# Kernel tuning notes

Measured on AMD Instinct MI355X. Metric: run time of the kernel, lower is better.

## Reference

```python
import jax, jax.numpy as jnp
import numpy as np

M_BIT = 8      # BfpConfig.bfp_M_Bit (sign + mantissa bits)
BLOCK = 64     # BFP block size along contraction (K) dim
K_SIZE, STRIDE, PAD = 3, 1, 1


def bfp_quantize(x, m_bit=M_BIT, block=BLOCK):
    """Block-floating-point quantize along last axis: per-block shared exponent
    from max-abs, m_bit-wide signed mantissa, then dequantize back to fp."""
    shape = x.shape
    xb = x.reshape(shape[:-1] + (shape[-1] // block, block))
    maxabs = jnp.max(jnp.abs(xb), axis=-1, keepdims=True)
    exp = jnp.floor(jnp.log2(jnp.maximum(maxabs, jnp.float32(1e-38))))
    scale = jnp.exp2(exp - (m_bit - 2))          # lsb weight for this block
    qmax = jnp.float32(2.0 ** (m_bit - 1) - 1)
    q = jnp.clip(jnp.round(xb / scale), -qmax - 1.0, qmax) * scale
    q = jnp.where(maxabs == 0.0, 0.0, q)
    return q.reshape(shape)


def im2col(x, k, s, p):
    """Torch Unfold ordering: columns flattened as (C, kh, kw). x: [N,C,H,W]."""
    N, C, H, W = x.shape
    Ho = (H + 2 * p - k) // s + 1
    Wo = (W + 2 * p - k) // s + 1
    xp = jnp.pad(x, ((0, 0), (0, 0), (p, p), (p, p)))
    rows = []
    for i in range(k):
        for j in range(k):
            rows.append(xp[:, :, i:i + s * Ho:s, j:j + s * Wo:s])  # [N,C,Ho,Wo]
    # [k*k, N, C, Ho, Wo] -> [N, C, k*k, Ho*Wo] -> [N, C*k*k, Ho*Wo]
    patches = jnp.stack(rows, axis=0).transpose(1, 2, 0, 3, 4)
    return patches.reshape(N, C * k * k, Ho * Wo), Ho, Wo


def setup_inputs() -> dict:
    key = jax.random.key(0)
    k1, k2, k3 = jax.random.split(key, 3)
    inputs = jax.random.normal(k1, (32, 128, 56, 56), dtype=jnp.float32)
    fan_in = 128 * K_SIZE * K_SIZE
    weight = jax.random.normal(k2, (256, 128, K_SIZE, K_SIZE), dtype=jnp.float32) / np.sqrt(fan_in)
    bias = jax.random.normal(k3, (256,), dtype=jnp.float32) * 0.01
    return {"inputs": inputs, "weight": weight, "bias": bias}


def reference(inputs, weight, bias):
    N = inputs.shape[0]
    C_out = weight.shape[0]
    cols, Ho, Wo = im2col(inputs, K_SIZE, STRIDE, PAD)      # [N, K, Ho*Wo]
    a = cols.transpose(0, 2, 1).reshape(-1, cols.shape[1])  # [N*Ho*Wo, K]
    w = weight.reshape(C_out, -1)                           # [C_out, K]
    qa = bfp_quantize(a)
    qw = bfp_quantize(w)
    out = qa @ qw.T + bias                                  # [N*Ho*Wo, C_out]
    out = out.reshape(N, Ho, Wo, C_out).transpose(0, 3, 1, 2)
    return out
```

## Files before the change

kernel.cpp:

```cpp
#include <hip/hip_runtime.h>

typedef short short8 __attribute__((ext_vector_type(8)));
typedef __bf16 bf16x8 __attribute__((ext_vector_type(8)));
typedef float floatx4 __attribute__((ext_vector_type(4)));

__device__ __forceinline__ float make_pow2(int e) {
  return __builtin_bit_cast(float, (unsigned)((e + 127) << 23));
}

__device__ __forceinline__ void barrier_lgkm() {
  asm volatile("s_waitcnt lgkmcnt(0)" ::: "memory");
  __builtin_amdgcn_sched_barrier(0);
  __builtin_amdgcn_s_barrier();
  asm volatile("" ::: "memory");
  __builtin_amdgcn_sched_barrier(0);
}

__global__ void quant_w_kernel(const float* __restrict__ w, unsigned short* __restrict__ qw) {
  int b = blockIdx.x;
  int ct = b / 18, kb = b - ct * 18;
  int L = threadIdx.x;
  int co = ct * 16 + (L & 15);
  int kq = L >> 4;
  const float* wr = w + co * 1152 + kb * 64 + kq * 8;
  float v[16];
  float a = 0.f;
  #pragma unroll
  for (int ks = 0; ks < 2; ++ks)
    #pragma unroll
    for (int j = 0; j < 8; ++j) {
      float t = wr[ks * 32 + j];
      v[ks * 8 + j] = t;
      a = fmaxf(a, fabsf(t));
    }
  a = fmaxf(a, __shfl_xor(a, 16));
  a = fmaxf(a, __shfl_xor(a, 32));
  short8 q0 = (short8)0, q1 = (short8)0;
  if (a > 0.f) {
    int e = (int)((__builtin_bit_cast(unsigned, a) >> 23) & 0xffu) - 127;
    if (e < -126) e = -126;
    float inv = make_pow2(6 - e);
    float s   = make_pow2(e - 6);
    #pragma unroll
    for (int u = 0; u < 16; ++u) {
      float r = rintf(v[u] * inv);
      r = fminf(fmaxf(r, -128.f), 127.f);
      float qq = r * s;
      unsigned short hb = (unsigned short)(__builtin_bit_cast(unsigned, qq) >> 16);
      if (u < 8) q0[u] = (short)hb; else q1[u - 8] = (short)hb;
    }
  }
  unsigned short* dst = qw + (size_t)(ct * 18 + kb) * 1024;
  *(short8*)(dst + L * 8) = q0;
  *(short8*)(dst + 512 + L * 8) = q1;
}

__global__ __launch_bounds__(512, 4) void conv_bfp_kernel(
    const float* __restrict__ in, const unsigned short* __restrict__ qw,
    const float* __restrict__ bias, float* __restrict__ out) {
  __shared__ unsigned short As[2][64 * 64];
  __shared__ float pmax[2][8][64];

  const int bid = blockIdx.x;
  const int mt = (bid & 7) * 196 + (bid >> 3);
  const int t = threadIdx.x;
  const int lane = t & 63;
  const int wave = __builtin_amdgcn_readfirstlane(t >> 6);

  const unsigned m = mt * 64u + lane;
  const unsigned nimg = m / 3136u;
  const unsigned py = m - nimg * 3136u;
  const int y = (int)(py / 56u);
  const int x = (int)(py - (unsigned)y * 56u);
  const int vbase = (int)((nimg * 401408u + (unsigned)y * 56u + (unsigned)x) * 4u);
  int vm = 0;
  #pragma unroll
  for (int i = 0; i < 3; ++i)
    #pragma unroll
    for (int j = 0; j < 3; ++j)
      if ((unsigned)(y + i - 1) < 56u && (unsigned)(x + j - 1) < 56u)
        vm |= 1 << (i * 3 + j);

  const int lr = lane & 15;
  const int lk = (lane >> 4) << 4;
  const int swz = (lr & 7) << 4;

  floatx4 acc[4][2] = {};

  auto gather = [&](float (&av)[8], int kb) {
    const int k0 = __builtin_amdgcn_readfirstlane(kb * 64 + wave * 8);
    #pragma unroll
    for (int u = 0; u < 8; ++u) {
      int k = k0 + u;
      int c = (int)((unsigned)k / 9u);
      int ij = k - c * 9;
      int soff = c * 3136 + (ij / 3) * 56 + (ij % 3) - 57;
      const char* pk = (const char*)in + (ptrdiff_t)soff * 4;
      float v = 0.f;
      if ((vm >> ij) & 1)
        v = *(const float*)(pk + vbase);
      av[u] = v;
    }
  };

  auto loadB = [&](bf16x8 (&bq)[2][2], int kb) {
    #pragma unroll
    for (int ks = 0; ks < 2; ++ks)
      #pragma unroll
      for (int fn = 0; fn < 2; ++fn) {
        int ct = wave * 2 + fn;
        bq[ks][fn] = __builtin_bit_cast(bf16x8, *(const short8*)(
            (const char*)qw + ((size_t)((ct * 18 + kb) * 2 + ks) * 64 + lane) * 16));
      }
  };

  auto lmax_store = [&](float (&av)[8], int kb) {
    float lm = 0.f;
    #pragma unroll
    for (int u = 0; u < 8; ++u) lm = fmaxf(lm, fabsf(av[u]));
    pmax[kb & 1][wave][lane] = lm;
  };

  auto quantWrite = [&](float (&av)[8], int kb) {
    const float* pb = &pmax[kb & 1][0][lane];
    float ma = 0.f;
    #pragma unroll
    for (int j = 0; j < 8; ++j) ma = fmaxf(ma, pb[j * 64]);
    short8 aq;
    if (ma > 0.f) {
      int e = (int)((__builtin_bit_cast(unsigned, ma) >> 23) & 0xffu) - 127;
      if (e < -126) e = -126;
      float inv = make_pow2(6 - e);
      float s   = make_pow2(e - 6);
      #pragma unroll
      for (int u = 0; u < 8; ++u) {
        float r = rintf(av[u] * inv);
        r = fminf(fmaxf(r, -128.f), 127.f);
        float q = r * s;
        aq[u] = (short)(unsigned short)(__builtin_bit_cast(unsigned, q) >> 16);
      }
    } else {
      aq = (short8)0;
    }
    char* arow = (char*)As[kb & 1] + lane * 128;
    *(short8*)(arow + ((wave * 16) ^ ((lane & 7) << 4))) = aq;
  };

  auto mfmaBlk = [&](bf16x8 (&bq)[2][2], int kb) {
    const char* abase = (const char*)As[kb & 1];
    __builtin_amdgcn_s_setprio(1);
    #pragma unroll
    for (int ks = 0; ks < 2; ++ks) {
      const int kbyte = (ks * 64 + lk) ^ swz;
      #pragma unroll
      for (int fm = 0; fm < 4; ++fm) {
        bf16x8 af = __builtin_bit_cast(bf16x8,
            *(const short8*)(abase + (fm * 16 + lr) * 128 + kbyte));
        #pragma unroll
        for (int fn = 0; fn < 2; ++fn)
          acc[fm][fn] = __builtin_amdgcn_mfma_f32_16x16x32_bf16(bq[ks][fn], af, acc[fm][fn], 0, 0, 0);
      }
    }
    __builtin_amdgcn_s_setprio(0);
  };

  float av0[8], av1[8];
  bf16x8 bqA[2][2], bqB[2][2];

  gather(av0, 0);
  loadB(bqA, 0);
  gather(av1, 1);
  lmax_store(av0, 0);
  lmax_store(av1, 1);
  barrier_lgkm();
  quantWrite(av0, 0);

  auto phase = [&](int kb, float (&avq)[8], float (&avg)[8],
                   bf16x8 (&bqc)[2][2], bf16x8 (&bqn)[2][2]) {
    barrier_lgkm();
    if (kb < 17) quantWrite(avq, kb + 1);
    if (kb < 16) gather(avg, kb + 2);
    if (kb < 17) loadB(bqn, kb + 1);
    mfmaBlk(bqc, kb);
    if (kb < 16) lmax_store(avg, kb + 2);
  };

  #pragma unroll 1
  for (int kb = 0; kb < 18; kb += 2) {
    phase(kb,     av1, av0, bqA, bqB);
    phase(kb + 1, av0, av1, bqB, bqA);
  }

  const unsigned ni = (mt * 64u) / 3136u;
  const unsigned pp0 = mt * 64u - ni * 3136u;
  float* obase = out + (size_t)ni * 802816u + pp0;
  const int cg = (lane >> 4) << 2;
  #pragma unroll
  for (int fn = 0; fn < 2; ++fn) {
    floatx4 bv = *(const floatx4*)&bias[wave * 32 + fn * 16 + cg];
    #pragma unroll
    for (int r = 0; r < 4; ++r) {
      int co = wave * 32 + fn * 16 + cg + r;
      float* orow = obase + (size_t)co * 3136u;
      #pragma unroll
      for (int fm = 0; fm < 4; ++fm)
        orow[fm * 16 + lr] = acc[fm][fn][r] + bv[r];
    }
  }
}

extern "C" void kernel_launch(void* const* d_in, const int* in_sizes, int n_in,
                              void* d_out, int out_size, void* d_ws, size_t ws_size,
                              hipStream_t stream) {
  const float* in   = (const float*)d_in[0];
  const float* w    = (const float*)d_in[1];
  const float* bias = (const float*)d_in[2];
  float* out = (float*)d_out;
  unsigned short* qw = (unsigned short*)d_ws;

  quant_w_kernel<<<288, 64, 0, stream>>>(w, qw);
  conv_bfp_kernel<<<1568, 512, 0, stream>>>(in, qw, bias, out);
}
```

Before: 130.6 us.

## Deepen pipeline to process two K-blocks per barrier with 4-stage LDS ring

Expands the LDS A-tile and partial-max buffers from double to quadruple buffering. Each barrier-separated super-phase now quantizes two K-blocks, gathers two blocks further ahead, and runs MFMAs on two blocks. The aim is to halve the number of workgroup barriers and give global gathers more time in flight. The cost is twice the LDS footprint and more live registers, which may reduce occupancy below the 4-workgroup launch bound.

```diff
diff --git a/kernel.cpp b/kernel.cpp
--- a/kernel.cpp
+++ b/kernel.cpp
@@ -58,8 +58,8 @@
 __global__ __launch_bounds__(512, 4) void conv_bfp_kernel(
     const float* __restrict__ in, const unsigned short* __restrict__ qw,
     const float* __restrict__ bias, float* __restrict__ out) {
-  __shared__ unsigned short As[2][64 * 64];
-  __shared__ float pmax[2][8][64];
+  __shared__ unsigned short As[4][64 * 64];
+  __shared__ float pmax[4][8][64];
 
   const int bid = blockIdx.x;
   const int mt = (bid & 7) * 196 + (bid >> 3);
@@ -118,11 +118,11 @@
     float lm = 0.f;
     #pragma unroll
     for (int u = 0; u < 8; ++u) lm = fmaxf(lm, fabsf(av[u]));
-    pmax[kb & 1][wave][lane] = lm;
+    pmax[kb & 3][wave][lane] = lm;
   };
 
   auto quantWrite = [&](float (&av)[8], int kb) {
-    const float* pb = &pmax[kb & 1][0][lane];
+    const float* pb = &pmax[kb & 3][0][lane];
     float ma = 0.f;
     #pragma unroll
     for (int j = 0; j < 8; ++j) ma = fmaxf(ma, pb[j * 64]);
@@ -142,12 +142,12 @@
     } else {
       aq = (short8)0;
     }
-    char* arow = (char*)As[kb & 1] + lane * 128;
+    char* arow = (char*)As[kb & 3] + lane * 128;
     *(short8*)(arow + ((wave * 16) ^ ((lane & 7) << 4))) = aq;
   };
 
   auto mfmaBlk = [&](bf16x8 (&bq)[2][2], int kb) {
-    const char* abase = (const char*)As[kb & 1];
+    const char* abase = (const char*)As[kb & 3];
     __builtin_amdgcn_s_setprio(1);
     #pragma unroll
     for (int ks = 0; ks < 2; ++ks) {
@@ -164,32 +164,32 @@
     __builtin_amdgcn_s_setprio(0);
   };
 
-  float av0[8], av1[8];
-  bf16x8 bqA[2][2], bqB[2][2];
-
-  gather(av0, 0);
-  loadB(bqA, 0);
-  gather(av1, 1);
-  lmax_store(av0, 0);
-  lmax_store(av1, 1);
+  auto superp = [&](int kb, float (&q0)[8], float (&q1)[8],
+                    float (&g0)[8], float (&g1)[8]) {
+    barrier_lgkm();
+    bf16x8 bq[2][2], bq2[2][2];
+    loadB(bq, kb);
+    if (kb + 2 < 18) { quantWrite(q0, kb + 2); quantWrite(q1, kb + 3); }
+    if (kb + 4 < 18) { gather(g0, kb + 4); gather(g1, kb + 5); }
+    loadB(bq2, kb + 1);
+    mfmaBlk(bq, kb);
+    if (kb + 4 < 18) { lmax_store(g0, kb + 4); lmax_store(g1, kb + 5); }
+    mfmaBlk(bq2, kb + 1);
+  };
+
+  float gA[8], gB[8], gC[8], gD[8];
+
+  gather(gA, 0); gather(gB, 1); gather(gC, 2); gather(gD, 3);
+  lmax_store(gA, 0); lmax_store(gB, 1); lmax_store(gC, 2); lmax_store(gD, 3);
   barrier_lgkm();
-  quantWrite(av0, 0);
-
-  auto phase = [&](int kb, float (&avq)[8], float (&avg)[8],
-                   bf16x8 (&bqc)[2][2], bf16x8 (&bqn)[2][2]) {
-    barrier_lgkm();
-    if (kb < 17) quantWrite(avq, kb + 1);
-    if (kb < 16) gather(avg, kb + 2);
-    if (kb < 17) loadB(bqn, kb + 1);
-    mfmaBlk(bqc, kb);
-    if (kb < 16) lmax_store(avg, kb + 2);
-  };
+  quantWrite(gA, 0); quantWrite(gB, 1);
 
   #pragma unroll 1
-  for (int kb = 0; kb < 18; kb += 2) {
-    phase(kb,     av1, av0, bqA, bqB);
-    phase(kb + 1, av0, av1, bqB, bqA);
+  for (int kb = 0; kb < 16; kb += 4) {
+    superp(kb,     gC, gD, gA, gB);
+    superp(kb + 2, gA, gB, gC, gD);
   }
+  superp(16, gC, gD, gA, gB);
 
   const unsigned ni = (mt * 64u) / 3136u;
   const unsigned pp0 = mt * 64u - ni * 3136u;
```

Result: faster. 125.9 us (-3.5%).
